# Kernel optimization log

Hardware: AMD Instinct MI355X
Metric: run time of the kernel (lower is better)

## Reference

```python
import jax, jax.numpy as jnp
import numpy as np

B, L, N, DM = 32, 12, 883, 64
DSP, DTP, H, HID, HOR = 128, 128, 4, 64, 12
E_SPA = 14128
ENC_LAYERS = 3
HIDDEN = 5 * HID  # 2*embed + node + tid + diw = 320


def _gat(x, es, et, W, a_s, a_d, bias, edge_att=None):
    # GATConv-style attention with optional per-edge info-bottleneck mask (gat_ib)
    n = x.shape[0]
    h = (x @ W).reshape(n, H, -1)            # [n,H,Dh]
    sc_s = (h * a_s).sum(-1)                 # [n,H]
    sc_d = (h * a_d).sum(-1)
    al = jax.nn.leaky_relu(sc_s[es] + sc_d[et], 0.2)   # [E,H]
    al = al - jax.ops.segment_max(al, et, num_segments=n)[et]
    ex = jnp.exp(al)
    a = ex / jax.ops.segment_sum(ex, et, num_segments=n)[et]
    if edge_att is not None:
        a = a * edge_att[:, None]
    out = jax.ops.segment_sum(a[..., None] * h[es], et, num_segments=n)
    return out.reshape(n, -1) + bias


def _gsat(x, ei, gat_p, ext_p):
    # GSAT: embed -> extractor MLP on edge endpoint pairs -> sigmoid edge att -> masked conv
    es, et = ei[0], ei[1]
    emb = _gat(x, es, et, *gat_p)
    w1, b1, w2, b2, w3, b3 = ext_p
    f = jnp.concatenate([emb[es], emb[et]], axis=-1)
    logit = (jax.nn.relu(jax.nn.relu(f @ w1 + b1) @ w2 + b2) @ w3 + b3)[:, 0]
    att = jax.nn.sigmoid(logit)  # eval-mode (no concrete-relaxation sampling)
    return _gat(x, es, et, *gat_p, edge_att=att)


def setup_inputs():
    key = jax.random.key(0)
    ks = iter(jax.random.split(key, 80))
    def nrm(shape, s=0.02):
        return jax.random.normal(next(ks), shape, jnp.float32) * s
    hist = jax.random.normal(next(ks), (B, L, N, 3), jnp.float32)
    tid = jax.random.randint(next(ks), (B, L, N), 0, 288).astype(jnp.float32)
    diw = jax.random.randint(next(ks), (B, L, N), 0, 7).astype(jnp.float32)
    hist = hist.at[..., 1].set(tid).at[..., 2].set(diw)
    ei_spa = jax.random.randint(next(ks), (2, E_SPA), 0, N).astype(jnp.int32)
    g = jnp.arange(L, dtype=jnp.int32)
    ei_temp = jnp.stack([jnp.repeat(g, L), jnp.tile(g, L)])  # dense lag x lag temporal graph
    inp = dict(history_data=hist, edge_idx_spa=ei_spa, edge_idx_temp=ei_temp)
    inp.update(
        node_emb=nrm((N, HID)), tid_emb=nrm((288, HID)), diw_emb=nrm((7, HID)),
        start_w=nrm((3, DM)), start_b=jnp.zeros((DM,), jnp.float32),
        ts_w=nrm((DM * L, HID)), ts_b=jnp.zeros((HID,), jnp.float32),
        tr_spat_w=nrm((L * DM, DSP)), tr_spat_b=jnp.zeros((DSP,), jnp.float32),
        inv_spat_w=nrm((DSP, L * DM)), inv_spat_b=jnp.zeros((L * DM,), jnp.float32),
        tr_temp_w=nrm((N * DM, DTP)), tr_temp_b=jnp.zeros((DTP,), jnp.float32),
        inv_temp_w=nrm((DTP, N * DM)), inv_temp_b=jnp.zeros((N * DM,), jnp.float32),
        gat_sp_w=nrm((DSP, DSP)), gat_sp_asrc=nrm((H, DSP // H)), gat_sp_adst=nrm((H, DSP // H)), gat_sp_bias=jnp.zeros((DSP,), jnp.float32),
        ext_sp_w1=nrm((2 * DSP, 4 * DSP)), ext_sp_b1=jnp.zeros((4 * DSP,), jnp.float32),
        ext_sp_w2=nrm((4 * DSP, DSP)), ext_sp_b2=jnp.zeros((DSP,), jnp.float32),
        ext_sp_w3=nrm((DSP, 1)), ext_sp_b3=jnp.zeros((1,), jnp.float32),
        gat_tp_w=nrm((DTP, DTP)), gat_tp_asrc=nrm((H, DTP // H)), gat_tp_adst=nrm((H, DTP // H)), gat_tp_bias=jnp.zeros((DTP,), jnp.float32),
        ext_tp_w1=nrm((2 * DTP, 4 * DTP)), ext_tp_b1=jnp.zeros((4 * DTP,), jnp.float32),
        ext_tp_w2=nrm((4 * DTP, DTP)), ext_tp_b2=jnp.zeros((DTP,), jnp.float32),
        ext_tp_w3=nrm((DTP, 1)), ext_tp_b3=jnp.zeros((1,), jnp.float32),
        enc_w1=nrm((ENC_LAYERS, HIDDEN, HIDDEN)), enc_b1=jnp.zeros((ENC_LAYERS, HIDDEN), jnp.float32),
        enc_w2=nrm((ENC_LAYERS, HIDDEN, HIDDEN)), enc_b2=jnp.zeros((ENC_LAYERS, HIDDEN), jnp.float32),
        reg_w=nrm((HIDDEN, HOR)), reg_b=jnp.zeros((HOR,), jnp.float32),
    )
    return inp


def reference(history_data, edge_idx_spa, edge_idx_temp, node_emb, tid_emb, diw_emb,
              start_w, start_b, ts_w, ts_b,
              tr_spat_w, tr_spat_b, inv_spat_w, inv_spat_b,
              tr_temp_w, tr_temp_b, inv_temp_w, inv_temp_b,
              gat_sp_w, gat_sp_asrc, gat_sp_adst, gat_sp_bias,
              ext_sp_w1, ext_sp_b1, ext_sp_w2, ext_sp_b2, ext_sp_w3, ext_sp_b3,
              gat_tp_w, gat_tp_asrc, gat_tp_adst, gat_tp_bias,
              ext_tp_w1, ext_tp_b1, ext_tp_w2, ext_tp_b2, ext_tp_w3, ext_tp_b3,
              enc_w1, enc_b1, enc_w2, enc_b2, reg_w, reg_b):
    b, l, n = history_data.shape[:3]
    tid = jax.lax.stop_gradient(history_data[:, -1, :, 1]).astype(jnp.int32)
    diw = jax.lax.stop_gradient(history_data[:, -1, :, 2]).astype(jnp.int32)
    X = history_data[..., :3] @ start_w + start_b           # [B,L,N,DM]
    res = X.transpose(0, 2, 1, 3).reshape(b, n, l * DM)      # [B,N,L*DM]
    ts_res = res @ ts_w + ts_b                               # conv1x1 over nodes == per-node linear
    gp_sp = (gat_sp_w, gat_sp_asrc, gat_sp_adst, gat_sp_bias)
    ep_sp = (ext_sp_w1, ext_sp_b1, ext_sp_w2, ext_sp_b2, ext_sp_w3, ext_sp_b3)
    gp_tp = (gat_tp_w, gat_tp_asrc, gat_tp_adst, gat_tp_bias)
    ep_tp = (ext_tp_w1, ext_tp_b1, ext_tp_w2, ext_tp_b2, ext_tp_w3, ext_tp_b3)
    # batch_st_gsat: per-sample spatial GSAT then temporal GSAT (vmapped instead of Python loop)
    spa_in = res @ tr_spat_w + tr_spat_b                     # [B,N,DSP]
    spa_out = jax.vmap(lambda xx: _gsat(xx, edge_idx_spa, gp_sp, ep_sp))(spa_in)
    spa_back = (spa_out @ inv_spat_w + inv_spat_b).reshape(b, n, l, DM).transpose(0, 2, 1, 3)
    temp_in = spa_back.reshape(b, l, n * DM) @ tr_temp_w + tr_temp_b   # [B,L,DTP]
    temp_out = jax.vmap(lambda xx: _gsat(xx, edge_idx_temp, gp_tp, ep_tp))(temp_in)
    temp_back = (temp_out @ inv_temp_w + inv_temp_b).reshape(b, l, n, DM)
    ts_temp = temp_back.transpose(0, 2, 1, 3).reshape(b, n, l * DM) @ ts_w + ts_b
    hid = jnp.concatenate([
        ts_res, ts_temp,
        jnp.broadcast_to(node_emb, (b, n, HID)),
        tid_emb[tid], diw_emb[diw],
    ], axis=-1)                                              # [B,N,320]
    for i in range(ENC_LAYERS):  # MLP_res: x + fc2(relu(fc1(x)))
        hid = hid + jax.nn.relu(hid @ enc_w1[i] + enc_b1[i]) @ enc_w2[i] + enc_b2[i]
    pred = hid @ reg_w + reg_b                               # [B,N,HOR]
    return pred.transpose(0, 2, 1)[..., None]                # [B,HOR,N,1]
```

## Files before the change

kernel.cpp:

```cpp
#include <hip/hip_runtime.h>
#include <hip/hip_bf16.h>
#include <cstdint>
#include <cstddef>

#define B_   32
#define L_   12
#define N_   883
#define DM_  64
#define E_SP 14128
#define E_TP 144
#define NT_  12
#define RBN  28256
#define RBL  384
#define LDM  768
#define NDM  56512

static inline int cdiv_h(int a, int b){ return (a+b-1)/b; }

__device__ __forceinline__ ushort f2bf(float f){
    unsigned u = __float_as_uint(f);
    unsigned lsb = (u >> 16) & 1u;
    u += 0x7fffu + lsb;
    return (ushort)(u >> 16);
}
__device__ __forceinline__ float bf2f(ushort h){
    return __uint_as_float(((unsigned)h) << 16);
}
__device__ __forceinline__ ushort f2h(float f){
    _Float16 h = (_Float16)f;
    ushort r; __builtin_memcpy(&r, &h, 2);
    return r;
}

typedef __bf16 bf16x8 __attribute__((ext_vector_type(8)));
typedef _Float16 f16x8 __attribute__((ext_vector_type(8)));
typedef _Float16 f16x2 __attribute__((ext_vector_type(2)));
typedef float  f32x4  __attribute__((ext_vector_type(4)));
typedef short  s16x2  __attribute__((ext_vector_type(2)));
union BF8 { bf16x8 v; ushort u[8]; unsigned w[4]; int4 i; };
union HF8 { f16x8 v; ushort u[8]; unsigned w[4]; int4 i; };

__device__ __forceinline__ unsigned pkrelu(unsigned x){
    s16x2 v;
    __builtin_memcpy(&v, &x, 4);
    s16x2 z = 0;
    v = __builtin_elementwise_max(v, z);
    unsigned r;
    __builtin_memcpy(&r, &v, 4);
    return r;
}
__device__ __forceinline__ unsigned pkaddh(unsigned x, unsigned y){
    f16x2 a, b;
    __builtin_memcpy(&a, &x, 4);
    __builtin_memcpy(&b, &y, 4);
    a = a + b;
    unsigned r;
    __builtin_memcpy(&r, &a, 4);
    return r;
}

__global__ void k_mkA(const float* __restrict__ sw, const float* __restrict__ sb,
                      const float* __restrict__ tsw, const float* __restrict__ tsb,
                      const float* __restrict__ trsp, const float* __restrict__ trspb,
                      float* __restrict__ A1, float* __restrict__ A2,
                      float* __restrict__ cb1, float* __restrict__ cb2)
{
    int idx = blockIdx.x*256 + threadIdx.x;
    if (idx < 36*64) {
        int k = idx >> 6, h = idx & 63;
        int l = k/3, c = k - l*3;
        float s = 0.f;
        #pragma unroll 8
        for (int d = 0; d < 64; ++d) s += sw[c*64+d]*tsw[(size_t)(l*64+d)*64 + h];
        A1[idx] = s;
    } else if (idx < 36*64 + 36*128) {
        int i = idx - 36*64;
        int k = i >> 7, p = i & 127;
        int l = k/3, c = k - l*3;
        float s = 0.f;
        #pragma unroll 8
        for (int d = 0; d < 64; ++d) s += sw[c*64+d]*trsp[(size_t)(l*64+d)*128 + p];
        A2[i] = s;
    } else if (idx < 36*64 + 36*128 + 64) {
        int h = idx - (36*64 + 36*128);
        float s = tsb[h];
        #pragma unroll 8
        for (int k = 0; k < 768; ++k) s += sb[k & 63]*tsw[(size_t)k*64 + h];
        cb1[h] = s;
    } else if (idx < 36*64 + 36*128 + 64 + 128) {
        int p = idx - (36*64 + 36*128 + 64);
        float s = trspb[p];
        #pragma unroll 8
        for (int k = 0; k < 768; ++k) s += sb[k & 63]*trsp[(size_t)k*128 + p];
        cb2[p] = s;
    }
}
__global__ void k_front(const float* __restrict__ hist, const float* __restrict__ A1,
                        const float* __restrict__ A2, const float* __restrict__ cb1,
                        const float* __restrict__ cb2, float* __restrict__ ts_res,
                        ushort* __restrict__ spa_in)
{
    int idx = blockIdx.x*256 + threadIdx.x;
    if (idx >= RBN*192) return;
    int bn = idx / 192, h = idx - bn*192;
    int b = bn / N_, n = bn - b*N_;
    const float* hp = hist + ((size_t)(b*L_)*N_ + n)*3;
    bool isTs = (h < 64);
    int hh = isTs ? h : (h - 64);
    int stride = isTs ? 64 : 128;
    const float* A = isTs ? (A1 + hh) : (A2 + hh);
    float acc = isTs ? cb1[hh] : cb2[hh];
    #pragma unroll
    for (int l = 0; l < 12; ++l) {
        float x0 = hp[l*2649 + 0];
        float x1 = hp[l*2649 + 1];
        float x2 = hp[l*2649 + 2];
        acc += x0*A[(l*3+0)*stride] + x1*A[(l*3+1)*stride] + x2*A[(l*3+2)*stride];
    }
    if (isTs) ts_res[(size_t)bn*64 + hh] = acc;
    else      spa_in[(size_t)bn*128 + hh] = f2bf(acc);
}

template<int CT, int AMODE, int EPI, bool RELU, bool RES>
__launch_bounds__(256)
__global__ void mgemm(const ushort* __restrict__ A, const ushort* __restrict__ WT,
                      const float* __restrict__ bias, float* __restrict__ resF,
                      void* __restrict__ outP, int M, int N, int K)
{
    const int t = threadIdx.x, wv = t >> 6, l = t & 63;
    const int lr = l & 15, lk = l >> 4;
    const int row0 = blockIdx.y*64 + wv*16;
    const int col0 = blockIdx.x * (CT*16);
    int arr = row0 + lr; if (arr >= M) arr = M-1;
    int ab = 0, an = 0;
    if (AMODE == 1) { ab = arr / N_; an = arr - ab*N_; }
    const ushort* ap = A + (size_t)arr*K + lk*8;
    f32x4 acc[CT] = {};
    for (int k0 = 0; k0 < K; k0 += 32) {
        BF8 af;
        if (AMODE == 0) af.i = *(const int4*)(ap + k0);
        else {
            int k = k0 + lk*8; int ll = k >> 6, d = k & 63;
            af.i = *(const int4*)(A + ((size_t)(ab*L_ + ll))*NDM + (size_t)an*64 + d);
        }
        #pragma unroll
        for (int ct = 0; ct < CT; ++ct) {
            BF8 bf; bf.i = *(const int4*)&WT[(size_t)(col0 + ct*16 + lr)*K + k0 + lk*8];
            acc[ct] = __builtin_amdgcn_mfma_f32_16x16x32_bf16(af.v, bf.v, acc[ct], 0, 0, 0);
        }
    }
    #pragma unroll
    for (int ct = 0; ct < CT; ++ct) {
        int c = col0 + ct*16 + lr;
        float bv = 0.f;
        if (EPI == 2) { if (bias && c < 12) bv = bias[c]; }
        else if (bias) bv = bias[c];
        #pragma unroll
        for (int g = 0; g < 4; ++g) {
            int r = row0 + lk*4 + g;
            if (r >= M) continue;
            float v = acc[ct][g] + bv;
            if (RELU) v = fmaxf(v, 0.f);
            if (RES) {
                v += resF[(size_t)r*N + c];
                resF[(size_t)r*N + c] = v;
            }
            if (EPI == 0) {
                ((ushort*)outP)[(size_t)r*N + c] = f2bf(v);
            } else if (EPI == 1) {
                ((float*)outP)[(size_t)r*N + c] = v;
            } else if (EPI == 2) {
                if (c < 12) {
                    int b = r / N_, n = r - (r/N_)*N_;
                    ((float*)outP)[((size_t)(b*L_ + c))*N_ + n] = v;
                }
            } else {
                int b = r / N_, n = r - (r/N_)*N_;
                ((ushort*)outP)[((size_t)(b*L_ + (c>>6)))*NDM + (size_t)n*64 + (c&63)] = f2bf(v);
            }
        }
    }
}

template<int RT, int CT, int EPI, bool RELU, bool RES>
__launch_bounds__(256)
__global__ void mgemm_rt(const ushort* __restrict__ A, const ushort* __restrict__ WT,
                         const float* __restrict__ bias, float* __restrict__ resF,
                         void* __restrict__ outP, int M, int N, int K)
{
    const int t = threadIdx.x, wv = t >> 6, l = t & 63;
    const int lr = l & 15, lk = l >> 4;
    const int rowbase = blockIdx.y*(4*RT*16) + wv*(RT*16);
    const int col0 = blockIdx.x * (CT*16);
    const ushort* ap[RT];
    #pragma unroll
    for (int rt = 0; rt < RT; ++rt) {
        int arr = rowbase + rt*16 + lr; if (arr >= M) arr = M-1;
        ap[rt] = A + (size_t)arr*K + lk*8;
    }
    f32x4 acc[RT][CT] = {};
    for (int k0 = 0; k0 < K; k0 += 32) {
        BF8 af[RT];
        #pragma unroll
        for (int rt = 0; rt < RT; ++rt) af[rt].i = *(const int4*)(ap[rt] + k0);
        #pragma unroll
        for (int ct = 0; ct < CT; ++ct) {
            BF8 bf; bf.i = *(const int4*)&WT[(size_t)(col0 + ct*16 + lr)*K + k0 + lk*8];
            #pragma unroll
            for (int rt = 0; rt < RT; ++rt)
                acc[rt][ct] = __builtin_amdgcn_mfma_f32_16x16x32_bf16(af[rt].v, bf.v,
                                                                     acc[rt][ct], 0, 0, 0);
        }
    }
    #pragma unroll
    for (int rt = 0; rt < RT; ++rt)
        #pragma unroll
        for (int ct = 0; ct < CT; ++ct) {
            int c = col0 + ct*16 + lr;
            float bv = bias ? bias[c] : 0.f;
            #pragma unroll
            for (int g = 0; g < 4; ++g) {
                int r = rowbase + rt*16 + lk*4 + g;
                if (r >= M) continue;
                float v = acc[rt][ct][g] + bv;
                if (RELU) v = fmaxf(v, 0.f);
                if (RES) {
                    v += resF[(size_t)r*N + c];
                    resF[(size_t)r*N + c] = v;
                }
                if (EPI == 0) {
                    ((ushort*)outP)[(size_t)r*N + c] = f2bf(v);
                } else if (EPI == 1) {
                    ((float*)outP)[(size_t)r*N + c] = v;
                } else if (EPI == 4) {
                    ((ushort*)outP)[(size_t)r*N + c] = f2h(v);
                } else {
                    int b = r / N_, n = r - (r/N_)*N_;
                    ((ushort*)outP)[((size_t)(b*L_ + (c>>6)))*NDM + (size_t)n*64 + (c&63)] = f2bf(v);
                }
            }
        }
}

#define TCH 1024
__launch_bounds__(256)
__global__ void temp_in_mfma(const ushort* __restrict__ AT, const ushort* __restrict__ WtT,
                             float* __restrict__ out)
{
    const int t = threadIdx.x, wv = t >> 6, l = t & 63;
    const int lr = l & 15, lk = l >> 4;
    const int row0 = blockIdx.y * 96;
    const int c0 = wv * 32;
    const int k0b = blockIdx.x * TCH;
    const int kend = (k0b + TCH < NDM) ? (k0b + TCH) : NDM;
    f32x4 acc[6][2] = {};
    for (int k0 = k0b; k0 < kend; k0 += 32) {
        BF8 b0, b1;
        b0.i = *(const int4*)&WtT[(size_t)(c0 + lr)*NDM + k0 + lk*8];
        b1.i = *(const int4*)&WtT[(size_t)(c0 + 16 + lr)*NDM + k0 + lk*8];
        #pragma unroll
        for (int m = 0; m < 6; ++m) {
            BF8 af; af.i = *(const int4*)&AT[(size_t)(row0 + m*16 + lr)*NDM + k0 + lk*8];
            acc[m][0] = __builtin_amdgcn_mfma_f32_16x16x32_bf16(af.v, b0.v, acc[m][0], 0, 0, 0);
            acc[m][1] = __builtin_amdgcn_mfma_f32_16x16x32_bf16(af.v, b1.v, acc[m][1], 0, 0, 0);
        }
    }
    #pragma unroll
    for (int m = 0; m < 6; ++m)
        #pragma unroll
        for (int ct = 0; ct < 2; ++ct) {
            int c = c0 + ct*16 + lr;
            #pragma unroll
            for (int g = 0; g < 4; ++g) {
                int r = row0 + m*16 + lk*4 + g;
                atomicAdd(&out[(size_t)r*128 + c], acc[m][ct][g]);
            }
        }
}

__launch_bounds__(256)
__global__ void k_tsTemp(const ushort* __restrict__ toutB, const ushort* __restrict__ itWT,
                         const float* __restrict__ itb, const ushort* __restrict__ tswT,
                         const float* __restrict__ tsb, float* __restrict__ ts_temp)
{
    __shared__ ushort sb[384*72];
    const int n = blockIdx.x;
    const int t = threadIdx.x, wv = t >> 6, l = t & 63;
    const int lr = l & 15, lk = l >> 4;
    {
        f32x4 acc1[6][4] = {};
        for (int k0 = 0; k0 < 128; k0 += 32) {
            BF8 bfr[4];
            #pragma unroll
            for (int ct = 0; ct < 4; ++ct)
                bfr[ct].i = *(const int4*)&itWT[(size_t)(n*64 + ct*16 + lr)*128 + k0 + lk*8];
            #pragma unroll
            for (int rt = 0; rt < 6; ++rt) {
                BF8 af; af.i = *(const int4*)&toutB[(size_t)(wv*96 + rt*16 + lr)*128 + k0 + lk*8];
                #pragma unroll
                for (int ct = 0; ct < 4; ++ct)
                    acc1[rt][ct] = __builtin_amdgcn_mfma_f32_16x16x32_bf16(af.v, bfr[ct].v,
                                                                          acc1[rt][ct], 0, 0, 0);
            }
        }
        #pragma unroll
        for (int rt = 0; rt < 6; ++rt)
            #pragma unroll
            for (int ct = 0; ct < 4; ++ct) {
                int d = ct*16 + lr;
                float bv = itb[n*64 + d];
                #pragma unroll
                for (int g = 0; g < 4; ++g) {
                    int r = wv*96 + rt*16 + lk*4 + g;
                    int bb = r / 12;
                    sb[r*72 + (d ^ ((bb & 7) << 3))] = f2bf(acc1[rt][ct][g] + bv);
                }
            }
    }
    __syncthreads();
    f32x4 acc2[2] = {};
    #pragma unroll 2
    for (int j = 0; j < 24; ++j) {
        BF8 bfm; bfm.i = *(const int4*)&tswT[(size_t)(wv*16 + lr)*768 + j*32 + lk*8];
        int lidx = j >> 1;
        int koff = (j & 1)*32 + lk*8;
        #pragma unroll
        for (int rt = 0; rt < 2; ++rt) {
            int bb = rt*16 + lr;
            BF8 af;
            af.v = *(const bf16x8*)&sb[(bb*12 + lidx)*72 + (koff ^ ((bb & 7) << 3))];
            acc2[rt] = __builtin_amdgcn_mfma_f32_16x16x32_bf16(af.v, bfm.v, acc2[rt], 0, 0, 0);
        }
    }
    {
        int h = wv*16 + lr;
        float bv = tsb[h];
        #pragma unroll
        for (int rt = 0; rt < 2; ++rt)
            #pragma unroll
            for (int g = 0; g < 4; ++g) {
                int bb = rt*16 + lk*4 + g;
                ts_temp[((size_t)bb*N_ + n)*64 + h] = acc2[rt][g] + bv;
            }
    }
}

__global__ void k_sc(const ushort* __restrict__ h, const float* __restrict__ as_,
                     const float* __restrict__ ad_, float* __restrict__ scs,
                     float* __restrict__ scd, int R)
{
    int r = blockIdx.x*256 + threadIdx.x;
    if (r >= R) return;
    const ushort* hr = h + (size_t)r*128;
    #pragma unroll
    for (int hh = 0; hh < 4; ++hh) {
        float ss = 0.f, sd = 0.f;
        #pragma unroll
        for (int k = 0; k < 32; ++k) {
            float hv = bf2f(hr[hh*32 + k]);
            ss += hv*as_[hh*32+k];
            sd += hv*ad_[hh*32+k];
        }
        scs[(size_t)r*4+hh] = ss;
        scd[(size_t)r*4+hh] = sd;
    }
}

__global__ void k_count(const int* __restrict__ ei, int E, int* __restrict__ counts){
    int e = blockIdx.x*256 + threadIdx.x;
    if (e < E) atomicAdd(&counts[ei[E + e]], 1);
}
__global__ void k_scan(const int* __restrict__ counts, int* __restrict__ off,
                       int* __restrict__ cur, int n)
{
    __shared__ int s[1024];
    int t = threadIdx.x;
    int v0 = (t < n) ? counts[t] : 0;
    s[t] = v0;
    __syncthreads();
    for (int o = 1; o < 1024; o <<= 1) {
        int v = (t >= o) ? s[t-o] : 0;
        __syncthreads();
        s[t] += v;
        __syncthreads();
    }
    if (t < n) {
        off[t+1] = s[t];
        cur[t] = s[t] - v0;
        if (t == 0) off[0] = 0;
    }
}
__global__ void k_fill(const int* __restrict__ ei, int E, int* __restrict__ cur,
                       int* __restrict__ lst){
    int e = blockIdx.x*256 + threadIdx.x;
    if (e < E) {
        int pos = atomicAdd(&cur[ei[E+e]], 1);
        lst[pos] = e;
    }
}

template<bool USE_ATT>
__global__ void k_gather(const ushort* __restrict__ h, const float* __restrict__ scs,
                         const float* __restrict__ scd, const float* __restrict__ att,
                         const int* __restrict__ ei, const int* __restrict__ off,
                         const int* __restrict__ lst, const float* __restrict__ bias,
                         ushort* __restrict__ out, int E, int NN)
{
    int bn = blockIdx.x*4 + (threadIdx.x >> 6);
    int b = bn / NN, n = bn - b*NN;
    int lane = threadIdx.x & 63;
    int c0 = lane*2;
    int hh = lane >> 4;
    float sd = scd[(size_t)bn*4 + hh];
    int o0 = off[n], o1 = off[n+1];
    float ax = 0.f, ay = 0.f, sa = 0.f;
    for (int i = o0; i < o1; ++i) {
        int e = lst[i];
        int s = ei[e];
        float al = scs[(size_t)(b*NN + s)*4 + hh] + sd;
        al = al > 0.f ? al : 0.2f*al;
        float ex = expf(al);
        sa += ex;
        float a = USE_ATT ? ex * att[(size_t)b*E + e] : ex;
        unsigned hv = *(const unsigned*)&h[((size_t)b*NN + s)*128 + c0];
        ax += a * __uint_as_float(hv << 16);
        ay += a * __uint_as_float(hv & 0xffff0000u);
    }
    float rn = (sa > 0.f) ? 1.f/sa : 0.f;
    ushort2 o2;
    o2.x = f2bf(ax*rn + bias[c0]);
    o2.y = f2bf(ay*rn + bias[c0+1]);
    *(ushort2*)&out[(size_t)bn*128 + c0] = o2;
}

__global__ void k_prepW2(const float* __restrict__ W2, ushort* __restrict__ W2T)
{
    int idx = blockIdx.x*256 + threadIdx.x;
    if (idx >= 512*128) return;
    int k = idx >> 7, c = idx & 127;
    W2T[(size_t)c*512 + k] = f2h(W2[idx]);
}
__global__ void k_prepT(const float* __restrict__ W, ushort* __restrict__ WT, int K, int N)
{
    int idx = blockIdx.x*256 + threadIdx.x;
    if (idx >= K*N) return;
    int k = idx / N, c = idx - k*N;
    WT[(size_t)c*K + k] = f2bf(W[idx]);
}
__global__ void k_prepWtT(const float* __restrict__ W, ushort* __restrict__ WT)
{
    __shared__ ushort tile[128][129];
    int k0 = blockIdx.x * 128;
    int t = threadIdx.x;
    for (int i = t; i < 128*128; i += 256) {
        int k = i >> 7, c = i & 127;
        int kk = k0 + k;
        tile[c][k] = (kk < NDM) ? f2bf(W[(size_t)kk*128 + c]) : (ushort)0;
    }
    __syncthreads();
    for (int i = t; i < 128*128; i += 256) {
        int c = i >> 7, k = i & 127;
        int kk = k0 + k;
        if (kk < NDM) WT[(size_t)c*NDM + kk] = tile[c][k];
    }
}
__global__ void k_prepT_big(const float* __restrict__ W, ushort* __restrict__ WT)
{
    __shared__ float tile[128][65];
    int c0 = blockIdx.x * 64;
    int t = threadIdx.x;
    for (int i = t; i < 128*64; i += 256) {
        int k = i >> 6, ci = i & 63;
        tile[k][ci] = W[(size_t)k*NDM + c0 + ci];
    }
    __syncthreads();
    for (int i = t; i < 64*128; i += 256) {
        int ci = i >> 7, k = i & 127;
        WT[(size_t)(c0 + ci)*128 + k] = f2bf(tile[k][ci]);
    }
}
__global__ void k_bcat(const float* __restrict__ b1, float* __restrict__ dst){
    int i = blockIdx.x*256 + threadIdx.x;
    if (i < 1024) dst[i] = (i < 512) ? b1[i] : 0.f;
}

template<bool SWZ>
__launch_bounds__(256, 3)
__global__ void ext2_mfma(const ushort* __restrict__ PQ, const ushort* __restrict__ W2T,
                          const float* __restrict__ b2, const float* __restrict__ w3,
                          const float* __restrict__ b3p, const int* __restrict__ ei,
                          const int* __restrict__ lst,
                          float* __restrict__ att, int E, int NN, int nblk)
{
    __shared__ ushort Bs[2][128*40];
    int bid = blockIdx.x;
    if (SWZ) {
        bid = (blockIdx.x & 7) * (gridDim.x >> 3) + (blockIdx.x >> 3);
        if (bid >= nblk) bid = nblk - 1;
    }
    const int t = threadIdx.x;
    const int wv = t >> 6, l = t & 63;
    const int lr = l & 15, lk = l >> 4;

    const ushort* pr[2]; const ushort* qr[2];
    int row0[2];
    #pragma unroll
    for (int rt = 0; rt < 2; ++rt) {
        row0[rt] = bid*128 + wv*32 + rt*16;
        int r = row0[rt] + lr;
        int b = (int)((unsigned)r / (unsigned)E), i = r - b*E;
        int e = lst[i];
        pr[rt] = PQ + ((size_t)b*NN + ei[e])*1024 + lk*8;
        qr[rt] = PQ + ((size_t)b*NN + ei[E+e])*1024 + 512 + lk*8;
    }
    const int sc = t >> 1, sh = (t & 1) * 16;
    const ushort* wsrc = W2T + (size_t)sc*512 + sh;
    ushort* wd0 = &Bs[0][sc*40 + sh];
    ushort* wd1 = &Bs[1][sc*40 + sh];

    {
        int4 a0 = *(const int4*)(wsrc);
        int4 a1 = *(const int4*)(wsrc + 8);
        *(int4*)wd0 = a0;
        *(int4*)(wd0 + 8) = a1;
    }
    HF8 pu[2], qu[2];
    #pragma unroll
    for (int rt = 0; rt < 2; ++rt) {
        pu[rt].i = *(const int4*)(pr[rt]);
        qu[rt].i = *(const int4*)(qr[rt]);
    }
    int4 bnA = *(const int4*)(wsrc + 32);
    int4 bnB = *(const int4*)(wsrc + 40);
    __syncthreads();

    f32x4 acc[2][8] = {};
    for (int kc = 0; kc < 16; ++kc) {
        const int cb = kc & 1;
        HF8 af[2];
        #pragma unroll
        for (int rt = 0; rt < 2; ++rt)
            #pragma unroll
            for (int j = 0; j < 4; ++j)
                af[rt].w[j] = pkrelu(pkaddh(pu[rt].w[j], qu[rt].w[j]));
        {
            int ka = (kc+1 < 15) ? kc+1 : 15;
            #pragma unroll
            for (int rt = 0; rt < 2; ++rt) {
                pu[rt].i = *(const int4*)(pr[rt] + ka*32);
                qu[rt].i = *(const int4*)(qr[rt] + ka*32);
            }
        }
        __builtin_amdgcn_s_setprio(1);
        #pragma unroll
        for (int ct = 0; ct < 8; ++ct) {
            HF8 bfm;
            bfm.v = *(const f16x8*)&Bs[cb][(ct*16 + lr)*40 + lk*8];
            #pragma unroll
            for (int rt = 0; rt < 2; ++rt)
                acc[rt][ct] = __builtin_amdgcn_mfma_f32_16x16x32_f16(af[rt].v, bfm.v,
                                                                    acc[rt][ct], 0, 0, 0);
        }
        __builtin_amdgcn_s_setprio(0);
        if (kc < 15) {
            ushort* wd = cb ? wd0 : wd1;
            *(int4*)wd = bnA;
            *(int4*)(wd + 8) = bnB;
        }
        {
            int kb = (kc+2 < 15) ? kc+2 : 15;
            bnA = *(const int4*)(wsrc + kb*32);
            bnB = *(const int4*)(wsrc + kb*32 + 8);
        }
        __syncthreads();
    }
    float b3 = b3p[0];
    #pragma unroll
    for (int rt = 0; rt < 2; ++rt) {
        float part[4] = {0.f,0.f,0.f,0.f};
        #pragma unroll
        for (int ct = 0; ct < 8; ++ct) {
            int c = ct*16 + lr;
            float b2v = b2[c], w3v = w3[c];
            #pragma unroll
            for (int g = 0; g < 4; ++g)
                part[g] += fmaxf(acc[rt][ct][g] + b2v, 0.f) * w3v;
        }
        #pragma unroll
        for (int m = 1; m < 16; m <<= 1)
            #pragma unroll
            for (int g = 0; g < 4; ++g)
                part[g] += __shfl_xor(part[g], m, 64);
        if (lr == 0) {
            #pragma unroll
            for (int g = 0; g < 4; ++g) {
                int rr = row0[rt] + lk*4 + g;
                int b = (int)((unsigned)rr / (unsigned)E), i = rr - b*E;
                int e = lst[i];
                att[(size_t)b*E + e] = 1.f/(1.f + expf(-(part[g] + b3)));
            }
        }
    }
}

__global__ void k_bias_fill(float* __restrict__ dst, const float* __restrict__ bias, int n){
    int i = blockIdx.x*256 + threadIdx.x;
    if (i < n) dst[i] = bias[i & 127];
}
__global__ void k_f2b(const float* __restrict__ src, ushort* __restrict__ dst, int n){
    int i = blockIdx.x*256 + threadIdx.x;
    if (i < n) dst[i] = f2bf(src[i]);
}

__global__ void k_hid(const float* __restrict__ ts_res, const float* __restrict__ ts_temp,
                      const float* __restrict__ node_emb, const float* __restrict__ tid_emb,
                      const float* __restrict__ diw_emb, const float* __restrict__ hist,
                      float* __restrict__ hid, ushort* __restrict__ hidB)
{
    int idx = blockIdx.x*256 + threadIdx.x;
    if (idx >= RBN*320) return;
    int r = idx / 320, c = idx - r*320;
    int b = r / N_, n = r - b*N_;
    float v;
    if (c < 64)        v = ts_res[(size_t)r*64 + c];
    else if (c < 128)  v = ts_temp[(size_t)r*64 + (c-64)];
    else if (c < 192)  v = node_emb[(size_t)n*64 + (c-128)];
    else if (c < 256) {
        int tid = (int)hist[((size_t)(b*L_ + (L_-1))*N_ + n)*3 + 1];
        v = tid_emb[(size_t)tid*64 + (c-192)];
    } else {
        int diw = (int)hist[((size_t)(b*L_ + (L_-1))*N_ + n)*3 + 2];
        v = diw_emb[(size_t)diw*64 + (c-256)];
    }
    hid[idx] = v;
    hidB[idx] = f2bf(v);
}

extern "C" void kernel_launch(void* const* d_in, const int* in_sizes, int n_in,
                              void* d_out, int out_size, void* d_ws, size_t ws_size,
                              hipStream_t stream)
{
    (void)in_sizes; (void)n_in; (void)out_size; (void)ws_size;
    const float* hist      = (const float*)d_in[0];
    const int*   ei_sp     = (const int*)  d_in[1];
    const int*   ei_tp     = (const int*)  d_in[2];
    const float* node_emb  = (const float*)d_in[3];
    const float* tid_emb   = (const float*)d_in[4];
    const float* diw_emb   = (const float*)d_in[5];
    const float* start_w   = (const float*)d_in[6];
    const float* start_b   = (const float*)d_in[7];
    const float* ts_w      = (const float*)d_in[8];
    const float* ts_b      = (const float*)d_in[9];
    const float* tr_spat_w = (const float*)d_in[10];
    const float* tr_spat_b = (const float*)d_in[11];
    const float* inv_spat_w= (const float*)d_in[12];
    const float* inv_spat_b= (const float*)d_in[13];
    const float* tr_temp_w = (const float*)d_in[14];
    const float* tr_temp_b = (const float*)d_in[15];
    const float* inv_temp_w= (const float*)d_in[16];
    const float* inv_temp_b= (const float*)d_in[17];
    const float* gat_sp_w  = (const float*)d_in[18];
    const float* gat_sp_as = (const float*)d_in[19];
    const float* gat_sp_ad = (const float*)d_in[20];
    const float* gat_sp_b  = (const float*)d_in[21];
    const float* ext_sp_w1 = (const float*)d_in[22];
    const float* ext_sp_b1 = (const float*)d_in[23];
    const float* ext_sp_w2 = (const float*)d_in[24];
    const float* ext_sp_b2 = (const float*)d_in[25];
    const float* ext_sp_w3 = (const float*)d_in[26];
    const float* ext_sp_b3 = (const float*)d_in[27];
    const float* gat_tp_w  = (const float*)d_in[28];
    const float* gat_tp_as = (const float*)d_in[29];
    const float* gat_tp_ad = (const float*)d_in[30];
    const float* gat_tp_b  = (const float*)d_in[31];
    const float* ext_tp_w1 = (const float*)d_in[32];
    const float* ext_tp_b1 = (const float*)d_in[33];
    const float* ext_tp_w2 = (const float*)d_in[34];
    const float* ext_tp_b2 = (const float*)d_in[35];
    const float* ext_tp_w3 = (const float*)d_in[36];
    const float* ext_tp_b3 = (const float*)d_in[37];
    const float* enc_w1    = (const float*)d_in[38];
    const float* enc_b1    = (const float*)d_in[39];
    const float* enc_w2    = (const float*)d_in[40];
    const float* enc_b2    = (const float*)d_in[41];
    const float* reg_w     = (const float*)d_in[42];
    const float* reg_b     = (const float*)d_in[43];
    float* out = (float*)d_out;

    size_t o = 0;
    char* wsb = (char*)d_ws;
    auto allocB = [&](size_t bytes) -> void* {
        void* p = wsb + o;
        o += (bytes + 255) & ~(size_t)255;
        return p;
    };
    void* bufA = allocB((size_t)RBN*768*2);
    void* bufB = allocB((size_t)RBN*768*2);
    void* bufC = allocB((size_t)RBN*512*2);
    void* bufD = allocB((size_t)RBN*320*2);
    float*  ts_res  = (float*)allocB((size_t)RBN*64*4);
    ushort* spaB    = (ushort*)allocB((size_t)RBN*128*2);
    ushort* hB      = (ushort*)allocB((size_t)RBN*128*2);
    float*  sc_s    = (float*)allocB((size_t)RBN*4*4);
    float*  sc_d    = (float*)allocB((size_t)RBN*4*4);
    float*  att     = (float*)allocB((size_t)B_*E_SP*4);
    ushort* embB    = (ushort*)allocB((size_t)RBN*128*2);
    int*    csr     = (int*)allocB(17024*4);
    float*  temp_in = (float*)allocB((size_t)RBL*128*4);
    ushort* tempB   = (ushort*)allocB((size_t)RBL*128*2);
    ushort* toutB   = (ushort*)allocB((size_t)RBL*128*2);
    ushort* PQ_t    = (ushort*)allocB((size_t)RBL*1024*2);
    float*  ts_temp = (float*)allocB((size_t)RBN*64*4);
    ushort* W2T_sp  = (ushort*)allocB(512*128*2);
    ushort* W2T_tp  = (ushort*)allocB(512*128*2);
    ushort* WtT     = (ushort*)allocB((size_t)128*NDM*2);
    ushort* itWT    = (ushort*)allocB((size_t)NDM*128*2);
    ushort* ispWT   = (ushort*)allocB(768*128*2);
    ushort* gspWT   = (ushort*)allocB(128*128*2);
    ushort* gtpWT   = (ushort*)allocB(128*128*2);
    ushort* w1catT_sp = (ushort*)allocB((size_t)1024*128*2);
    ushort* w1catT_tp = (ushort*)allocB((size_t)1024*128*2);
    float*  b1cat_sp  = (float*)allocB(1024*4);
    float*  b1cat_tp  = (float*)allocB(1024*4);
    ushort* w1T_enc = (ushort*)allocB((size_t)3*320*320*2);
    ushort* w2T_enc = (ushort*)allocB((size_t)3*320*320*2);
    ushort* tswT_hi = (ushort*)allocB(64*768*2);
    ushort* reg_wT  = (ushort*)allocB(16*320*2);
    float*  A1      = (float*)allocB(36*64*4);
    float*  A2      = (float*)allocB(36*128*4);
    float*  cb1     = (float*)allocB(64*4);
    float*  cb2     = (float*)allocB(128*4);

    ushort* AT    = (ushort*)bufA;
    float*  hid   = (float*)bufA;
    ushort* PQ_sp = (ushort*)bufB;
    ushort* hidB  = (ushort*)bufC;
    ushort* R1b   = (ushort*)bufD;

    int* counts_sp = csr;
    int* off_sp    = csr + 883;
    int* cur_sp    = csr + 1767;
    int* list_sp   = csr + 2650;
    int* counts_tp = csr + 16778;
    int* off_tp    = csr + 16790;
    int* cur_tp    = csr + 16803;
    int* list_tp   = csr + 16815;

    hipMemsetAsync(counts_sp, 0, 883*4, stream);
    k_count<<<cdiv_h(E_SP,256),256,0,stream>>>(ei_sp, E_SP, counts_sp);
    k_scan<<<1,1024,0,stream>>>(counts_sp, off_sp, cur_sp, 883);
    k_fill<<<cdiv_h(E_SP,256),256,0,stream>>>(ei_sp, E_SP, cur_sp, list_sp);
    hipMemsetAsync(counts_tp, 0, 12*4, stream);
    k_count<<<1,256,0,stream>>>(ei_tp, E_TP, counts_tp);
    k_scan<<<1,1024,0,stream>>>(counts_tp, off_tp, cur_tp, 12);
    k_fill<<<1,256,0,stream>>>(ei_tp, E_TP, cur_tp, list_tp);
    k_mkA<<<cdiv_h(36*64+36*128+192,256),256,0,stream>>>(start_w, start_b, ts_w, ts_b,
                                                         tr_spat_w, tr_spat_b,
                                                         A1, A2, cb1, cb2);
    k_prepW2<<<cdiv_h(512*128,256),256,0,stream>>>(ext_sp_w2, W2T_sp);
    k_prepW2<<<cdiv_h(512*128,256),256,0,stream>>>(ext_tp_w2, W2T_tp);
    k_prepWtT<<<cdiv_h(NDM,128),256,0,stream>>>(tr_temp_w, WtT);
    k_prepT_big<<<NDM/64,256,0,stream>>>(inv_temp_w, itWT);
    k_prepT<<<cdiv_h(128*768,256),256,0,stream>>>(inv_spat_w, ispWT, 128, 768);
    k_prepT<<<cdiv_h(128*128,256),256,0,stream>>>(gat_sp_w, gspWT, 128, 128);
    k_prepT<<<cdiv_h(128*128,256),256,0,stream>>>(gat_tp_w, gtpWT, 128, 128);
    k_prepT<<<cdiv_h(128*512,256),256,0,stream>>>(ext_sp_w1,           w1catT_sp,           128, 512);
    k_prepT<<<cdiv_h(128*512,256),256,0,stream>>>(ext_sp_w1 + 128*512, w1catT_sp + 512*128, 128, 512);
    k_prepT<<<cdiv_h(128*512,256),256,0,stream>>>(ext_tp_w1,           w1catT_tp,           128, 512);
    k_prepT<<<cdiv_h(128*512,256),256,0,stream>>>(ext_tp_w1 + 128*512, w1catT_tp + 512*128, 128, 512);
    k_bcat<<<4,256,0,stream>>>(ext_sp_b1, b1cat_sp);
    k_bcat<<<4,256,0,stream>>>(ext_tp_b1, b1cat_tp);
    for (int i = 0; i < 3; ++i) {
        k_prepT<<<cdiv_h(320*320,256),256,0,stream>>>(enc_w1 + (size_t)i*320*320, w1T_enc + (size_t)i*320*320, 320, 320);
        k_prepT<<<cdiv_h(320*320,256),256,0,stream>>>(enc_w2 + (size_t)i*320*320, w2T_enc + (size_t)i*320*320, 320, 320);
    }
    k_prepT<<<cdiv_h(768*64,256),256,0,stream>>>(ts_w, tswT_hi, 768, 64);
    hipMemsetAsync(reg_wT, 0, 16*320*2, stream);
    k_prepT<<<cdiv_h(320*12,256),256,0,stream>>>(reg_w, reg_wT, 320, 12);

    k_front<<<cdiv_h(RBN*192,256),256,0,stream>>>(hist, A1, A2, cb1, cb2, ts_res, spaB);

    mgemm_rt<2,4,0,false,false><<<dim3(2,221),256,0,stream>>>(spaB, gspWT, nullptr, nullptr,
                                                              hB, RBN, 128, 128);
    k_sc<<<cdiv_h(RBN,256),256,0,stream>>>(hB, gat_sp_as, gat_sp_ad, sc_s, sc_d, RBN);
    k_gather<false><<<RBN/4,256,0,stream>>>(hB, sc_s, sc_d, nullptr, ei_sp, off_sp, list_sp,
                                            gat_sp_b, embB, E_SP, N_);
    mgemm_rt<2,8,4,false,false><<<dim3(8,221),256,0,stream>>>(embB, w1catT_sp, b1cat_sp, nullptr,
                                                              PQ_sp, RBN, 1024, 128);
    ext2_mfma<true><<<3536,256,0,stream>>>(PQ_sp, W2T_sp, ext_sp_b2, ext_sp_w3, ext_sp_b3,
                                           ei_sp, list_sp, att, E_SP, N_, (B_*E_SP)/128);
    k_gather<true><<<RBN/4,256,0,stream>>>(hB, sc_s, sc_d, att, ei_sp, off_sp, list_sp,
                                           gat_sp_b, spaB, E_SP, N_);

    mgemm_rt<2,4,3,false,false><<<dim3(12,221),256,0,stream>>>(spaB, ispWT, inv_spat_b, nullptr,
                                                               AT, RBN, 768, 128);
    k_bias_fill<<<cdiv_h(RBL*128,256),256,0,stream>>>(temp_in, tr_temp_b, RBL*128);
    temp_in_mfma<<<dim3(56,4),256,0,stream>>>(AT, WtT, temp_in);
    k_f2b<<<cdiv_h(RBL*128,256),256,0,stream>>>(temp_in, tempB, RBL*128);

    mgemm_rt<2,4,0,false,false><<<dim3(2,3),256,0,stream>>>(tempB, gtpWT, nullptr, nullptr,
                                                            hB, RBL, 128, 128);
    k_sc<<<cdiv_h(RBL,256),256,0,stream>>>(hB, gat_tp_as, gat_tp_ad, sc_s, sc_d, RBL);
    k_gather<false><<<RBL/4,256,0,stream>>>(hB, sc_s, sc_d, nullptr, ei_tp, off_tp, list_tp,
                                            gat_tp_b, embB, E_TP, NT_);
    mgemm_rt<2,8,4,false,false><<<dim3(8,3),256,0,stream>>>(embB, w1catT_tp, b1cat_tp, nullptr,
                                                            PQ_t, RBL, 1024, 128);
    ext2_mfma<false><<<(B_*E_TP)/128,256,0,stream>>>(PQ_t, W2T_tp, ext_tp_b2, ext_tp_w3,
                                                     ext_tp_b3, ei_tp, list_tp, att, E_TP, NT_,
                                                     (B_*E_TP)/128);
    k_gather<true><<<RBL/4,256,0,stream>>>(hB, sc_s, sc_d, att, ei_tp, off_tp, list_tp,
                                           gat_tp_b, toutB, E_TP, NT_);

    k_tsTemp<<<N_,256,0,stream>>>(toutB, itWT, inv_temp_b, tswT_hi, ts_b, ts_temp);

    k_hid<<<cdiv_h(RBN*320,256),256,0,stream>>>(ts_res, ts_temp, node_emb, tid_emb, diw_emb, hist,
                                                hid, hidB);
    for (int i = 0; i < 3; ++i) {
        mgemm_rt<2,5,0,true,false><<<dim3(4,221),256,0,stream>>>(hidB, w1T_enc + (size_t)i*320*320,
                                                                 enc_b1 + i*320, nullptr, R1b, RBN, 320, 320);
        mgemm_rt<2,5,0,false,true><<<dim3(4,221),256,0,stream>>>(R1b, w2T_enc + (size_t)i*320*320,
                                                                 enc_b2 + i*320, hid, hidB, RBN, 320, 320);
    }
    mgemm<1,0,2,false,false><<<dim3(1,442),256,0,stream>>>(hidB, reg_wT, reg_b, nullptr,
                                                           out, RBN, 16, 320);
}
```

Baseline: 1.232 ms.

## Fuse inverse-spatial projection into temporal input GEMM via shared-memory tiles

Replaces the separate inv_spat GEMM (writing a large bf16 AT intermediate to global memory) plus the temporal-input split-K GEMM with one kernel. Each block computes the inverse spatial projection for a chunk of nodes into an XOR-swizzled LDS tile and immediately feeds it into the temporal projection, accumulating into the output with atomics. This removes the global write and re-read of the ~43MB intermediate, at the cost of a smaller grid (222 blocks), per-node syncthreads, and more atomics.

After: 1.218 ms. Within noise of the previous version (-1.2%).

```diff
diff --git a/kernel.cpp b/kernel.cpp
--- a/kernel.cpp
+++ b/kernel.cpp
@@ -242,38 +242,73 @@
         }
 }
 
-#define TCH 1024
+#define TNC 8
 __launch_bounds__(256)
-__global__ void temp_in_mfma(const ushort* __restrict__ AT, const ushort* __restrict__ WtT,
-                             float* __restrict__ out)
-{
+__global__ void k_tempIn(const ushort* __restrict__ spaB, const ushort* __restrict__ ispWT,
+                         const float* __restrict__ isb, const ushort* __restrict__ WtT,
+                         float* __restrict__ out)
+{
+    __shared__ ushort T1[16*768];
     const int t = threadIdx.x, wv = t >> 6, l = t & 63;
     const int lr = l & 15, lk = l >> 4;
-    const int row0 = blockIdx.y * 96;
-    const int c0 = wv * 32;
-    const int k0b = blockIdx.x * TCH;
-    const int kend = (k0b + TCH < NDM) ? (k0b + TCH) : NDM;
-    f32x4 acc[6][2] = {};
-    for (int k0 = k0b; k0 < kend; k0 += 32) {
-        BF8 b0, b1;
-        b0.i = *(const int4*)&WtT[(size_t)(c0 + lr)*NDM + k0 + lk*8];
-        b1.i = *(const int4*)&WtT[(size_t)(c0 + 16 + lr)*NDM + k0 + lk*8];
-        #pragma unroll
-        for (int m = 0; m < 6; ++m) {
-            BF8 af; af.i = *(const int4*)&AT[(size_t)(row0 + m*16 + lr)*NDM + k0 + lk*8];
-            acc[m][0] = __builtin_amdgcn_mfma_f32_16x16x32_bf16(af.v, b0.v, acc[m][0], 0, 0, 0);
-            acc[m][1] = __builtin_amdgcn_mfma_f32_16x16x32_bf16(af.v, b1.v, acc[m][1], 0, 0, 0);
+    const int bh = blockIdx.y;
+    const int n0 = blockIdx.x * TNC;
+    const int nEnd = (n0 + TNC < N_) ? n0 + TNC : N_;
+
+    f32x4 acc2[3][8] = {};
+    for (int n = n0; n < nEnd; ++n) {
+        f32x4 acc1[12] = {};
+        for (int k0 = 0; k0 < 128; k0 += 32) {
+            BF8 af; af.i = *(const int4*)&spaB[((size_t)(bh*16 + lr)*N_ + n)*128 + k0 + lk*8];
+            #pragma unroll
+            for (int ct = 0; ct < 12; ++ct) {
+                BF8 bf; bf.i = *(const int4*)&ispWT[(size_t)(wv*192 + ct*16 + lr)*128 + k0 + lk*8];
+                acc1[ct] = __builtin_amdgcn_mfma_f32_16x16x32_bf16(af.v, bf.v, acc1[ct], 0, 0, 0);
+            }
+        }
+        __syncthreads();
+        #pragma unroll
+        for (int ct = 0; ct < 12; ++ct) {
+            int c = wv*192 + ct*16 + lr;
+            float bv = isb[c];
+            int ll = c >> 6, d = c & 63;
+            #pragma unroll
+            for (int g = 0; g < 4; ++g) {
+                int b = lk*4 + g;
+                int r = b*12 + ll;
+                T1[b*768 + ll*64 + (d ^ ((r & 7) << 3))] = f2bf(acc1[ct][g] + bv);
+            }
+        }
+        __syncthreads();
+        #pragma unroll
+        for (int kc = 0; kc < 2; ++kc) {
+            BF8 bfr[8];
+            #pragma unroll
+            for (int ct = 0; ct < 8; ++ct)
+                bfr[ct].i = *(const int4*)&WtT[(size_t)(ct*16 + lr)*NDM + (size_t)n*64 + kc*32 + lk*8];
+            #pragma unroll
+            for (int rt = 0; rt < 3; ++rt) {
+                int r = wv*48 + rt*16 + lr;
+                int b = r / 12, ll = r - b*12;
+                int k = kc*32 + lk*8;
+                BF8 af;
+                af.v = *(const bf16x8*)&T1[b*768 + ll*64 + (k ^ ((r & 7) << 3))];
+                #pragma unroll
+                for (int ct = 0; ct < 8; ++ct)
+                    acc2[rt][ct] = __builtin_amdgcn_mfma_f32_16x16x32_bf16(af.v, bfr[ct].v,
+                                                                          acc2[rt][ct], 0, 0, 0);
+            }
         }
     }
     #pragma unroll
-    for (int m = 0; m < 6; ++m)
-        #pragma unroll
-        for (int ct = 0; ct < 2; ++ct) {
-            int c = c0 + ct*16 + lr;
+    for (int rt = 0; rt < 3; ++rt)
+        #pragma unroll
+        for (int ct = 0; ct < 8; ++ct) {
+            int p = ct*16 + lr;
             #pragma unroll
             for (int g = 0; g < 4; ++g) {
-                int r = row0 + m*16 + lk*4 + g;
-                atomicAdd(&out[(size_t)r*128 + c], acc[m][ct][g]);
+                int r = bh*192 + wv*48 + rt*16 + lk*4 + g;
+                atomicAdd(&out[(size_t)r*128 + p], acc2[rt][ct][g]);
             }
         }
 }
@@ -731,7 +766,6 @@
     float*  cb1     = (float*)allocB(64*4);
     float*  cb2     = (float*)allocB(128*4);
 
-    ushort* AT    = (ushort*)bufA;
     float*  hid   = (float*)bufA;
     ushort* PQ_sp = (ushort*)bufB;
     ushort* hidB  = (ushort*)bufC;
@@ -792,10 +826,8 @@
     k_gather<true><<<RBN/4,256,0,stream>>>(hB, sc_s, sc_d, att, ei_sp, off_sp, list_sp,
                                            gat_sp_b, spaB, E_SP, N_);
 
-    mgemm_rt<2,4,3,false,false><<<dim3(12,221),256,0,stream>>>(spaB, ispWT, inv_spat_b, nullptr,
-                                                               AT, RBN, 768, 128);
     k_bias_fill<<<cdiv_h(RBL*128,256),256,0,stream>>>(temp_in, tr_temp_b, RBL*128);
-    temp_in_mfma<<<dim3(56,4),256,0,stream>>>(AT, WtT, temp_in);
+    k_tempIn<<<dim3(cdiv_h(N_,TNC),2),256,0,stream>>>(spaB, ispWT, inv_spat_b, WtT, temp_in);
     k_f2b<<<cdiv_h(RBL*128,256),256,0,stream>>>(temp_in, tempB, RBL*128);
 
     mgemm_rt<2,4,0,false,false><<<dim3(2,3),256,0,stream>>>(tempB, gtpWT, nullptr, nullptr,
```
